# Kernel tuning notes

Measured on AMD Instinct MI355X. Metric: run time of the kernel, lower is better.

Reference implementation:

```python
import jax, jax.numpy as jnp
import numpy as np

EMBED_DIM = 1024
NUM_HEADS = 16
HEAD_DIM = EMBED_DIM // NUM_HEADS


def setup_inputs() -> dict:
    key = jax.random.key(0)
    k_x, k_wqkv, k_bqkv, k_wout, k_bout = jax.random.split(key, 5)
    s = 1.0 / np.sqrt(EMBED_DIM)
    return {
        "x": jax.random.normal(k_x, (2, 2048, EMBED_DIM), dtype=jnp.float32),
        "w_qkv": jax.random.uniform(k_wqkv, (EMBED_DIM, 3 * EMBED_DIM), jnp.float32, -s, s),
        "b_qkv": jax.random.uniform(k_bqkv, (3 * EMBED_DIM,), jnp.float32, -s, s),
        "w_out": jax.random.uniform(k_wout, (EMBED_DIM, EMBED_DIM), jnp.float32, -s, s),
        "b_out": jax.random.uniform(k_bout, (EMBED_DIM,), jnp.float32, -s, s),
    }


def reference(x, w_qkv, b_qkv, w_out, b_out):
    B, S, D = x.shape
    H, Hd = NUM_HEADS, HEAD_DIM
    # qkv projection, then per-head chunk: layout matches torch view(B,S,H,3*Hd).chunk(3,-1)
    qkv = (x @ w_qkv + b_qkv).reshape(B, S, H, 3, Hd)  # [B,S,H,3,Hd]
    q = qkv[..., 0, :]  # [B,S,H,Hd]
    k = qkv[..., 1, :]
    v = qkv[..., 2, :]
    scale = 1.0 / np.sqrt(Hd).astype(np.float32)
    scores = jnp.einsum("bqhd,bkhd->bhqk", q, k) * scale  # [B,H,S,S]
    probs = jax.nn.softmax(scores, axis=-1)
    out = jnp.einsum("bhqk,bkhd->bqhd", probs, v).reshape(B, S, D)
    return out @ w_out + b_out
```

## Files before the change

### kernel.cpp

```cpp
#include <hip/hip_runtime.h>
#include <hip/hip_bf16.h>


typedef __bf16 bf16;
typedef __bf16 bf16x8 __attribute__((ext_vector_type(8)));
typedef float  f32x4  __attribute__((ext_vector_type(4)));
typedef float  f32x16 __attribute__((ext_vector_type(16)));
typedef unsigned int uint;
typedef unsigned int uint2v __attribute__((ext_vector_type(2)));

__device__ __forceinline__ void gload_lds16(const void* g, void* l) {
  __builtin_amdgcn_global_load_lds(
      (const __attribute__((address_space(1))) unsigned int*)g,
      (__attribute__((address_space(3))) unsigned int*)l, 16, 0, 0);
}

__device__ __forceinline__ uint pkbf16(float lo, float hi) {
  union { bf16 h[2]; uint u; } t;
  t.h[0] = (bf16)lo; t.h[1] = (bf16)hi;
  return t.u;
}

__device__ __forceinline__ void pl32swapu(uint& a, uint& b) {
  uint2v r = __builtin_amdgcn_permlane32_swap(a, b, false, false);
  a = r.x; b = r.y;
}
__device__ __forceinline__ void pl32swapf(float& a, float& b) {
  uint ua = __builtin_bit_cast(uint, a), ub = __builtin_bit_cast(uint, b);
  pl32swapu(ua, ub);
  a = __builtin_bit_cast(float, ua); b = __builtin_bit_cast(float, ub);
}

__global__ __launch_bounds__(256) void k_prep(const float* __restrict__ x,
                                              const float* __restrict__ w_qkv,
                                              const float* __restrict__ w_out,
                                              bf16* __restrict__ xb,
                                              bf16* __restrict__ wqT,
                                              bf16* __restrict__ woT) {
  __shared__ float tile[32][33];
  const int b = blockIdx.x;
  const int tid = threadIdx.x;
  if (b < 2048) {
    int i = (b * 256 + tid) * 8;
    float4 a = *(const float4*)(x + i);
    float4 c = *(const float4*)(x + i + 4);
    bf16x8 o;
    o[0] = (bf16)a.x; o[1] = (bf16)a.y; o[2] = (bf16)a.z; o[3] = (bf16)a.w;
    o[4] = (bf16)c.x; o[5] = (bf16)c.y; o[6] = (bf16)c.z; o[7] = (bf16)c.w;
    *(bf16x8*)(xb + i) = o;
    return;
  }
  const bool perm = (b < 5120);
  const float* in = perm ? w_qkv : w_out;
  bf16* out = perm ? wqT : woT;
  const int N = perm ? 3072 : 1024;
  int idx = perm ? (b - 2048) : (b - 5120);
  int gx = perm ? (idx % 96) : (idx % 32);
  int gy = perm ? (idx / 96) : (idx / 32);
  int n0 = gx * 32, k0 = gy * 32;
  int tx = tid & 31, ty = tid >> 5;
#pragma unroll
  for (int i = 0; i < 4; i++)
    tile[ty + i * 8][tx] = in[(size_t)(k0 + ty + i * 8) * N + n0 + tx];
  __syncthreads();
#pragma unroll
  for (int i = 0; i < 4; i++) {
    int n = n0 + ty + i * 8;
    int row = n;
    if (perm) {
      int rem = n % 192;
      row = (rem >> 6) * 1024 + (n / 192) * 64 + (rem & 63);
    }
    out[(size_t)row * 1024 + k0 + tx] = (bf16)tile[tx][ty + i * 8];
  }
}

template<int BM, int BN>
__device__ __forceinline__ void gemm_tile(const bf16* __restrict__ A, const bf16* __restrict__ B,
                                          int K, int m0, int n0,
                                          bf16* As, bf16* Bs, f32x4 acc[BM / 32][BN / 32]) {
  const int tid  = threadIdx.x;
  const int lane = tid & 63;
  const int wr   = (tid >> 7) & 1;
  const int wc   = (tid >> 6) & 1;
  constexpr int LA = BM / 64, LB = BN / 64;
  auto stage = [&](int k0v, int b) {
#pragma unroll
    for (int i = 0; i < LA; i++) {
      int row = i * 64 + (tid >> 2);
      int sw  = (tid & 3) ^ (row & 3);
      gload_lds16(A + (size_t)(m0 + row) * K + k0v + sw * 8, (char*)As + b * (BM * 64) + i * 4096 + tid * 16);
    }
#pragma unroll
    for (int i = 0; i < LB; i++) {
      int row = i * 64 + (tid >> 2);
      int sw  = (tid & 3) ^ (row & 3);
      gload_lds16(B + (size_t)(n0 + row) * K + k0v + sw * 8, (char*)Bs + b * (BN * 64) + i * 4096 + tid * 16);
    }
  };
  const int nk = K / 32;
  stage(0, 0); stage(32, 1); stage(64, 2);
  for (int t = 0; t < nk; t++) {
    if (t < nk - 2) {
      if constexpr (LA + LB == 4) asm volatile("s_waitcnt vmcnt(8)" ::: "memory");
      else                        asm volatile("s_waitcnt vmcnt(6)" ::: "memory");
    } else if (t < nk - 1) {
      if constexpr (LA + LB == 4) asm volatile("s_waitcnt vmcnt(4)" ::: "memory");
      else                        asm volatile("s_waitcnt vmcnt(3)" ::: "memory");
    } else {
      asm volatile("s_waitcnt vmcnt(0)" ::: "memory");
    }
    __builtin_amdgcn_s_barrier();
    asm volatile("" ::: "memory");
    if (t + 3 < nk) stage((t + 3) * 32, (t + 3) & 3);
    const int cur = t & 3;
    bf16x8 af[BM / 32], bfr[BN / 32];
#pragma unroll
    for (int r = 0; r < BM / 32; r++) {
      int ra = wr * (BM / 2) + r * 16 + (lane & 15);
      af[r]  = *(const bf16x8*)((const char*)As + cur * (BM * 64) + ra * 64 + ((((lane >> 4) << 4)) ^ ((ra & 3) << 4)));
    }
#pragma unroll
    for (int c = 0; c < BN / 32; c++) {
      int rb = wc * (BN / 2) + c * 16 + (lane & 15);
      bfr[c] = *(const bf16x8*)((const char*)Bs + cur * (BN * 64) + rb * 64 + ((((lane >> 4) << 4)) ^ ((rb & 3) << 4)));
    }
#pragma unroll
    for (int r = 0; r < BM / 32; r++)
#pragma unroll
      for (int c = 0; c < BN / 32; c++)
        acc[r][c] = __builtin_amdgcn_mfma_f32_16x16x32_bf16(af[r], bfr[c], acc[r][c], 0, 0, 0);
    asm volatile("" ::: "memory");
  }
}

__global__ __launch_bounds__(512, 2) void k_gemm_qkv(const bf16* __restrict__ A, const bf16* __restrict__ Bt,
                                                     const float* __restrict__ bias,
                                                     bf16* __restrict__ qb, bf16* __restrict__ kb,
                                                     bf16* __restrict__ vtb) {
  __shared__ char GS[131072];
  const int tid  = threadIdx.x;
  const int lane = tid & 63;
  const int wave = tid >> 6;
  const int wr   = wave >> 2;
  const int wc   = wave & 3;
  const int m0 = blockIdx.x * 256, n0 = blockIdx.y * 256;
  const int K = 1024;

  f32x4 acc[8][4];
  f32x4 zero = {0.f, 0.f, 0.f, 0.f};
#pragma unroll
  for (int ms = 0; ms < 8; ms++)
#pragma unroll
    for (int ns = 0; ns < 4; ns++) acc[ms][ns] = zero;

  const int ccs = tid & 7;
  int rA[2], rB[2];
  {
    int lr0 = tid >> 3;
    rA[0] = lr0;
    rB[0] = (lr0 & 31) + ((lr0 >> 5) << 6);
    int lr1 = 64 + lr0;
    rA[1] = (lr1 & 63) + 128;
    rB[1] = (lr1 & 31) + ((lr1 >> 5) << 6);
  }
  const bf16* Agp[2]; const bf16* Bgp[2];
  int Alo[2], Blo[2];
#pragma unroll
  for (int j = 0; j < 2; j++) {
    Agp[j] = A  + (size_t)(m0 + rA[j]) * K + (ccs ^ (rA[j] & 7)) * 8;
    Alo[j] = rA[j] * 128 + ccs * 16;
    Bgp[j] = Bt + (size_t)(n0 + rB[j]) * K + (ccs ^ (rB[j] & 7)) * 8;
    Blo[j] = rB[j] * 128 + ccs * 16;
  }
  auto stA = [&](int t, int h) {
    int b = t & 1;
#pragma unroll
    for (int j = 0; j < 2; j++)
      gload_lds16(Agp[j] + (size_t)(h * 64) * K + t * 64, GS + b * 32768 + Alo[j] + h * 8192);
  };
  auto stB = [&](int t, int h) {
    int b = t & 1;
#pragma unroll
    for (int j = 0; j < 2; j++)
      gload_lds16(Bgp[j] + (size_t)(h * 32) * K + t * 64, GS + 65536 + b * 32768 + Blo[j] + h * 4096);
  };

  bf16x8 af[4][2], bf0[2][2], bf1[2][2];
  auto rdA = [&](const char* Ab, int mh) {
#pragma unroll
    for (int ms = 0; ms < 4; ms++)
#pragma unroll
      for (int ks = 0; ks < 2; ks++) {
        int row = wr * 128 + (mh * 4 + ms) * 16 + (lane & 15);
        int ch = (ks * 4 + (lane >> 4)) ^ (row & 7);
        af[ms][ks] = *(const bf16x8*)(Ab + row * 128 + ch * 16);
      }
  };
  auto rdB = [&](const char* Bb, int nh, bf16x8 (&bfx)[2][2]) {
#pragma unroll
    for (int ns = 0; ns < 2; ns++)
#pragma unroll
      for (int ks = 0; ks < 2; ks++) {
        int row = wc * 64 + (nh * 2 + ns) * 16 + (lane & 15);
        int ch = (ks * 4 + (lane >> 4)) ^ (row & 7);
        bfx[ns][ks] = *(const bf16x8*)(Bb + row * 128 + ch * 16);
      }
  };
  auto mm = [&](int mh, int nh, bf16x8 (&bfx)[2][2]) {
    __builtin_amdgcn_s_setprio(1);
#pragma unroll
    for (int ks = 0; ks < 2; ks++)
#pragma unroll
      for (int ms = 0; ms < 4; ms++)
#pragma unroll
        for (int ns = 0; ns < 2; ns++)
          acc[mh * 4 + ms][nh * 2 + ns] =
              __builtin_amdgcn_mfma_f32_16x16x32_bf16(af[ms][ks], bfx[ns][ks],
                                                      acc[mh * 4 + ms][nh * 2 + ns], 0, 0, 0);
    __builtin_amdgcn_s_setprio(0);
  };

#define BARRIER do { asm volatile("" ::: "memory"); __builtin_amdgcn_s_barrier(); \
                     asm volatile("" ::: "memory"); } while (0)

  stA(0, 0); stB(0, 0); stB(0, 1); stA(0, 1);
  stA(1, 0); stB(1, 0); stB(1, 1);
  asm volatile("s_waitcnt vmcnt(6)" ::: "memory");
  __builtin_amdgcn_s_barrier();
  asm volatile("" ::: "memory");

  for (int I = 0; I < 8; I++) {
    const int T = 2 * I;
    const char* Ab0 = GS;
    const char* Bb0 = GS + 65536;
    const char* Ab1 = GS + 32768;
    const char* Bb1 = GS + 65536 + 32768;
    const bool m2 = (T + 2 < 16), m3 = (T + 3 < 16);

    rdA(Ab0, 0); rdB(Bb0, 0, bf0);
    stA(T + 1, 1);
    BARRIER;
    mm(0, 0, bf0);

    rdB(Bb0, 1, bf1);
    if (m2) stA(T + 2, 0);
    BARRIER;
    mm(0, 1, bf1);

    rdA(Ab0, 1);
    if (m2) stB(T + 2, 0);
    BARRIER;
    mm(1, 0, bf0);

    if (m2) {
      stB(T + 2, 1);
      asm volatile("s_waitcnt vmcnt(6)" ::: "memory");
    } else {
      asm volatile("s_waitcnt vmcnt(0)" ::: "memory");
    }
    __builtin_amdgcn_s_barrier();
    asm volatile("" ::: "memory");
    mm(1, 1, bf1);

    rdA(Ab1, 0); rdB(Bb1, 0, bf0);
    if (m2) stA(T + 2, 1);
    BARRIER;
    mm(0, 0, bf0);

    rdB(Bb1, 1, bf1);
    if (m3) stA(T + 3, 0);
    BARRIER;
    mm(0, 1, bf1);

    rdA(Ab1, 1);
    if (m3) stB(T + 3, 0);
    BARRIER;
    mm(1, 0, bf0);

    if (m3) {
      stB(T + 3, 1);
      asm volatile("s_waitcnt vmcnt(6)" ::: "memory");
    } else {
      asm volatile("s_waitcnt vmcnt(0)" ::: "memory");
    }
    __builtin_amdgcn_s_barrier();
    asm volatile("" ::: "memory");
    mm(1, 1, bf1);
  }
#undef BARRIER

  const int group = n0 >> 10;
  const int hb = (n0 & 1023) >> 6;
  const int b_ = m0 >> 11;
  const float QSs = 0.125f * 1.4426950408889634f;
  char* TL = GS;

  if (group < 2) {
#pragma unroll
    for (int ms = 0; ms < 8; ms++) {
      int mloc = wr * 128 + ms * 16 + ((lane >> 4) << 2);
#pragma unroll
      for (int ns = 0; ns < 4; ns++) {
        int nloc = wc * 64 + ns * 16 + (lane & 15);
        int np = n0 + nloc;
        float bv = bias[((np & 1023) >> 6) * 192 + group * 64 + (np & 63)];
#pragma unroll
        for (int g = 0; g < 4; g++) {
          float v = acc[ms][ns][g] + bv;
          if (group == 0) v *= QSs;
          int m = mloc + g;
          int byte = m * 512 + ((((nloc >> 3) ^ (m & 7)) << 4) | ((nloc & 7) << 1));
          *(bf16*)(TL + byte) = (bf16)v;
        }
      }
    }
    __syncthreads();
    bf16* dst = (group == 0) ? qb : kb;
#pragma unroll
    for (int it = 0; it < 16; it++) {
      int cid = it * 512 + tid;
      int row = cid >> 5, cc = cid & 31;
      int hh = hb + (cc >> 3), ck = cc & 7;
      bf16x8 v8 = *(const bf16x8*)(TL + row * 512 + ((cc ^ (row & 7)) << 4));
      *(bf16x8*)(dst + ((size_t)(b_ * 16 + hh) * 2048 + (m0 & 2047) + row) * 64 + ck * 8) = v8;
    }
  } else {
#pragma unroll
    for (int ms = 0; ms < 8; ms++) {
      int mloc = wr * 128 + ms * 16 + ((lane >> 4) << 2);
#pragma unroll
      for (int ns = 0; ns < 4; ns++) {
        int nloc = wc * 64 + ns * 16 + (lane & 15);
        int np = n0 + nloc;
        float bv = bias[((np & 1023) >> 6) * 192 + 2 * 64 + (np & 63)];
#pragma unroll
        for (int g = 0; g < 4; g++) {
          float v = acc[ms][ns][g] + bv;
          int m = mloc + g;
          int byte = nloc * 512 + ((((m >> 3) ^ (nloc & 7)) << 4) | ((m & 7) << 1));
          *(bf16*)(TL + byte) = (bf16)v;
        }
      }
    }
    __syncthreads();
#pragma unroll
    for (int it = 0; it < 16; it++) {
      int cid = it * 512 + tid;
      int row = cid >> 5, mc = cid & 31;
      int hh = hb + (row >> 6), dd = row & 63;
      bf16x8 v8 = *(const bf16x8*)(TL + row * 512 + ((mc ^ (row & 7)) << 4));
      *(bf16x8*)(vtb + ((size_t)(b_ * 16 + hh) * 64 + dd) * 2048 + (m0 & 2047) + mc * 8) = v8;
    }
  }
}

__global__ __launch_bounds__(256) void k_gemm_out(const bf16* __restrict__ A, const bf16* __restrict__ Bt,
                                                  const float* __restrict__ bias,
                                                  float* __restrict__ out) {
  __shared__ bf16 As[4 * 64 * 32];
  __shared__ bf16 Bs[4 * 128 * 32];
  int m0 = blockIdx.x * 64, n0 = blockIdx.y * 128;
  f32x4 zero = {0.f, 0.f, 0.f, 0.f};
  f32x4 acc[2][4];
#pragma unroll
  for (int r = 0; r < 2; r++)
#pragma unroll
    for (int c = 0; c < 4; c++) acc[r][c] = zero;
  gemm_tile<64, 128>(A, Bt, 1024, m0, n0, As, Bs, acc);
  const int lane = threadIdx.x & 63;
  const int wr = (threadIdx.x >> 7) & 1, wc = (threadIdx.x >> 6) & 1;
#pragma unroll
  for (int r = 0; r < 2; r++) {
    int mbase = m0 + wr * 32 + r * 16 + ((lane >> 4) << 2);
#pragma unroll
    for (int c = 0; c < 4; c++) {
      int n = n0 + wc * 64 + c * 16 + (lane & 15);
      float bv = bias[n];
#pragma unroll
      for (int g = 0; g < 4; g++)
        out[(size_t)(mbase + g) * 1024 + n] = acc[r][c][g] + bv;
    }
  }
}

__global__ __launch_bounds__(512, 2) void k_attn(const bf16* __restrict__ qb, const bf16* __restrict__ kb,
                                                 const bf16* __restrict__ vtb, bf16* __restrict__ ob) {
  __shared__ char SMEM[73728];
  const int tid  = threadIdx.x;
  const int lane = tid & 63;
  const int wave = tid >> 6;
  const int qp   = wave & 3;
  const int half = wave >> 2;
  const int ln31 = lane & 31;
  const int g    = lane >> 5;

  int l = blockIdx.x;
  int x = l & 7, j = l >> 3;
  int qt = j & 7;
  int bh = x * 4 + (j >> 3);

  const int q0 = qt * 256 + qp * 64;

  bf16x8 qfa[4], qfb[4];
  {
    const bf16* qpa = qb + ((size_t)bh * 2048 + q0 + ln31) * 64 + g * 8;
    const bf16* qpb = qb + ((size_t)bh * 2048 + q0 + 32 + ln31) * 64 + g * 8;
#pragma unroll
    for (int dc = 0; dc < 4; dc++) {
      qfa[dc] = *(const bf16x8*)(qpa + dc * 16);
      qfb[dc] = *(const bf16x8*)(qpb + dc * 16);
    }
  }

  const f32x16 z16 = 0.f;
  f32x16 Oa0 = 0.f, Oa1 = 0.f, Ob0 = 0.f, Ob1 = 0.f;
  float lacc_a[4] = {0.f, 0.f, 0.f, 0.f};
  float lacc_b[4] = {0.f, 0.f, 0.f, 0.f};

  const int rbo = ln31 * 144 + (g << 4);
  const char* kbs0 = SMEM + half * 9216 + rbo;
  const char* kbs1 = SMEM + 36864 + half * 9216 + rbo;
  const char* vbs0 = SMEM + 18432 + half * 9216 + rbo;
  const char* vbs1 = SMEM + 36864 + 18432 + half * 9216 + rbo;

  const int c1 = tid, r1 = c1 / 9, cc1 = c1 % 9;
  const int of1 = (cc1 == 8 ? 0 : cc1) * 8;
  const bf16* kg0a = kb  + ((size_t)bh * 2048 +        r1) * 64 + of1;
  const bf16* kg1a = kb  + ((size_t)bh * 2048 + 1024 + r1) * 64 + of1;
  const bf16* vg0a = vtb + ((size_t)bh * 64 + r1) * 2048 +        of1;
  const bf16* vg1a = vtb + ((size_t)bh * 64 + r1) * 2048 + 1024 + of1;
  const int se = tid >> 6;
  const int ce = 512 + (tid & 63), re = ce / 9, cce = ce % 9;
  const int ofe = (cce == 8 ? 0 : cce) * 8;
  const bf16* gext =
      (se == 0) ? kb  + ((size_t)bh * 2048 +        re) * 64 + ofe :
      (se == 1) ? kb  + ((size_t)bh * 2048 + 1024 + re) * 64 + ofe :
      (se == 2) ? vtb + ((size_t)bh * 64 + re) * 2048 +        ofe :
                  vtb + ((size_t)bh * 64 + re) * 2048 + 1024 + ofe;
  const size_t gadv = (se < 2) ? 4096 : 64;
  const int eoff = se * 9216 + ce * 16;

  auto stage = [&](int t, int s) {
    char* bs = SMEM + s * 36864;
    gload_lds16(kg0a + (size_t)t * 4096, bs +         c1 * 16);
    gload_lds16(kg1a + (size_t)t * 4096, bs + 9216  + c1 * 16);
    gload_lds16(vg0a + t * 64,           bs + 18432 + c1 * 16);
    gload_lds16(vg1a + t * 64,           bs + 27648 + c1 * 16);
    if (tid < 256) gload_lds16(gext + (size_t)t * gadv, bs + eoff);
  };

  auto smx = [&](f32x16& sv, bf16x8& f0, bf16x8& f1, float (&lc)[4]) {
#pragma unroll
    for (int r = 0; r < 16; r++) sv[r] = __builtin_amdgcn_exp2f(sv[r]);
#pragma unroll
    for (int r = 0; r < 4; r++)
      lc[r] += (sv[r] + sv[r + 4]) + (sv[r + 8] + sv[r + 12]);
    uint a0 = pkbf16(sv[0], sv[1]), a1 = pkbf16(sv[2], sv[3]);
    uint a2 = pkbf16(sv[4], sv[5]), a3 = pkbf16(sv[6], sv[7]);
    pl32swapu(a0, a2); pl32swapu(a1, a3);
    union { uint w[4]; bf16x8 v; } pa;
    pa.w[0] = a0; pa.w[1] = a1; pa.w[2] = a2; pa.w[3] = a3;
    f0 = pa.v;
    uint b0 = pkbf16(sv[8], sv[9]),  b1 = pkbf16(sv[10], sv[11]);
    uint b2 = pkbf16(sv[12], sv[13]), b3 = pkbf16(sv[14], sv[15]);
    pl32swapu(b0, b2); pl32swapu(b1, b3);
    union { uint w[4]; bf16x8 v; } pb;
    pb.w[0] = b0; pb.w[1] = b1; pb.w[2] = b2; pb.w[3] = b3;
    f1 = pb.v;
  };

  stage(0, 0);
  for (int t = 0; t < 16; t++) {
    asm volatile("s_waitcnt vmcnt(0)" ::: "memory");
    __builtin_amdgcn_s_barrier();
    asm volatile("" ::: "memory");
    if (t + 1 < 16) stage(t + 1, (t + 1) & 1);

    const char* Kb = (t & 1) ? kbs1 : kbs0;
    const char* Vb = (t & 1) ? vbs1 : vbs0;

    f32x16 sAa, sAb, sBa, sBb;
    __builtin_amdgcn_s_setprio(1);
    {
      bf16x8 kA = *(const bf16x8*)(Kb + 0);
      bf16x8 kB = *(const bf16x8*)(Kb + 4608);
      sAa = __builtin_amdgcn_mfma_f32_32x32x16_bf16(kA, qfa[0], z16, 0, 0, 0);
      sAb = __builtin_amdgcn_mfma_f32_32x32x16_bf16(kA, qfb[0], z16, 0, 0, 0);
      sBa = __builtin_amdgcn_mfma_f32_32x32x16_bf16(kB, qfa[0], z16, 0, 0, 0);
      sBb = __builtin_amdgcn_mfma_f32_32x32x16_bf16(kB, qfb[0], z16, 0, 0, 0);
    }
#pragma unroll
    for (int dc = 1; dc < 4; dc++) {
      bf16x8 kA = *(const bf16x8*)(Kb + dc * 32);
      bf16x8 kB = *(const bf16x8*)(Kb + 4608 + dc * 32);
      sAa = __builtin_amdgcn_mfma_f32_32x32x16_bf16(kA, qfa[dc], sAa, 0, 0, 0);
      sAb = __builtin_amdgcn_mfma_f32_32x32x16_bf16(kA, qfb[dc], sAb, 0, 0, 0);
      sBa = __builtin_amdgcn_mfma_f32_32x32x16_bf16(kB, qfa[dc], sBa, 0, 0, 0);
      sBb = __builtin_amdgcn_mfma_f32_32x32x16_bf16(kB, qfb[dc], sBb, 0, 0, 0);
    }
    __builtin_amdgcn_s_setprio(0);

    bf16x8 fa0, fa1, fb0, fb1;
    smx(sAa, fa0, fa1, lacc_a);
    smx(sAb, fb0, fb1, lacc_b);
    __builtin_amdgcn_s_setprio(1);
    {
      bf16x8 v0 = *(const bf16x8*)(Vb + 0);
      bf16x8 v1 = *(const bf16x8*)(Vb + 4608);
      Oa0 = __builtin_amdgcn_mfma_f32_32x32x16_bf16(v0, fa0, Oa0, 0, 0, 0);
      Ob0 = __builtin_amdgcn_mfma_f32_32x32x16_bf16(v0, fb0, Ob0, 0, 0, 0);
      Oa1 = __builtin_amdgcn_mfma_f32_32x32x16_bf16(v1, fa0, Oa1, 0, 0, 0);
      Ob1 = __builtin_amdgcn_mfma_f32_32x32x16_bf16(v1, fb0, Ob1, 0, 0, 0);
      v0 = *(const bf16x8*)(Vb + 32);
      v1 = *(const bf16x8*)(Vb + 4640);
      Oa0 = __builtin_amdgcn_mfma_f32_32x32x16_bf16(v0, fa1, Oa0, 0, 0, 0);
      Ob0 = __builtin_amdgcn_mfma_f32_32x32x16_bf16(v0, fb1, Ob0, 0, 0, 0);
      Oa1 = __builtin_amdgcn_mfma_f32_32x32x16_bf16(v1, fa1, Oa1, 0, 0, 0);
      Ob1 = __builtin_amdgcn_mfma_f32_32x32x16_bf16(v1, fb1, Ob1, 0, 0, 0);
    }
    __builtin_amdgcn_s_setprio(0);
    smx(sBa, fa0, fa1, lacc_a);
    smx(sBb, fb0, fb1, lacc_b);
    __builtin_amdgcn_s_setprio(1);
    {
      bf16x8 v0 = *(const bf16x8*)(Vb + 64);
      bf16x8 v1 = *(const bf16x8*)(Vb + 4672);
      Oa0 = __builtin_amdgcn_mfma_f32_32x32x16_bf16(v0, fa0, Oa0, 0, 0, 0);
      Ob0 = __builtin_amdgcn_mfma_f32_32x32x16_bf16(v0, fb0, Ob0, 0, 0, 0);
      Oa1 = __builtin_amdgcn_mfma_f32_32x32x16_bf16(v1, fa0, Oa1, 0, 0, 0);
      Ob1 = __builtin_amdgcn_mfma_f32_32x32x16_bf16(v1, fb0, Ob1, 0, 0, 0);
      v0 = *(const bf16x8*)(Vb + 96);
      v1 = *(const bf16x8*)(Vb + 4704);
      Oa0 = __builtin_amdgcn_mfma_f32_32x32x16_bf16(v0, fa1, Oa0, 0, 0, 0);
      Ob0 = __builtin_amdgcn_mfma_f32_32x32x16_bf16(v0, fb1, Ob0, 0, 0, 0);
      Oa1 = __builtin_amdgcn_mfma_f32_32x32x16_bf16(v1, fa1, Oa1, 0, 0, 0);
      Ob1 = __builtin_amdgcn_mfma_f32_32x32x16_bf16(v1, fb1, Ob1, 0, 0, 0);
    }
    __builtin_amdgcn_s_setprio(0);
    asm volatile("" ::: "memory");
  }

  float l_ra = (lacc_a[0] + lacc_a[1]) + (lacc_a[2] + lacc_a[3]);
  { float o = l_ra; pl32swapf(l_ra, o); l_ra += o; }
  float l_rb = (lacc_b[0] + lacc_b[1]) + (lacc_b[2] + lacc_b[3]);
  { float o = l_rb; pl32swapf(l_rb, o); l_rb += o; }

  float* Opart = (float*)SMEM;
  float* LsA   = (float*)(SMEM + 69632);
  float* LsB   = (float*)(SMEM + 70144);
  __syncthreads();
  if (half == 1) {
    float* my = Opart + (qp * 64 + lane) * 68;
#pragma unroll
    for (int c = 0; c < 4; c++) {
      *(f32x4*)(my +      c * 4) = f32x4{Oa0[c*4], Oa0[c*4+1], Oa0[c*4+2], Oa0[c*4+3]};
      *(f32x4*)(my + 16 + c * 4) = f32x4{Oa1[c*4], Oa1[c*4+1], Oa1[c*4+2], Oa1[c*4+3]};
      *(f32x4*)(my + 32 + c * 4) = f32x4{Ob0[c*4], Ob0[c*4+1], Ob0[c*4+2], Ob0[c*4+3]};
      *(f32x4*)(my + 48 + c * 4) = f32x4{Ob1[c*4], Ob1[c*4+1], Ob1[c*4+2], Ob1[c*4+3]};
    }
    if (lane < 32) { LsA[qp * 32 + ln31] = l_ra; LsB[qp * 32 + ln31] = l_rb; }
  }
  __syncthreads();
  float inva = 0.f, invb = 0.f;
  if (half == 0) {
    const float* pr = Opart + (qp * 64 + lane) * 68;
#pragma unroll
    for (int c = 0; c < 4; c++) {
      f32x4 a0 = *(const f32x4*)(pr +      c * 4);
      f32x4 a1 = *(const f32x4*)(pr + 16 + c * 4);
      f32x4 b0 = *(const f32x4*)(pr + 32 + c * 4);
      f32x4 b1 = *(const f32x4*)(pr + 48 + c * 4);
#pragma unroll
      for (int k = 0; k < 4; k++) {
        Oa0[c*4+k] += a0[k]; Oa1[c*4+k] += a1[k];
        Ob0[c*4+k] += b0[k]; Ob1[c*4+k] += b1[k];
      }
    }
    inva = 1.0f / (l_ra + LsA[qp * 32 + ln31]);
    invb = 1.0f / (l_rb + LsB[qp * 32 + ln31]);
  }
  __syncthreads();
  bf16 (*Os)[64][72] = reinterpret_cast<bf16 (*)[64][72]>(SMEM);
  if (half == 0) {
#pragma unroll
    for (int r = 0; r < 16; r++) {
      int d0 = (r & 3) + 8 * (r >> 2) + 4 * g;
      Os[qp][ln31][d0]           = (bf16)(Oa0[r] * inva);
      Os[qp][ln31][d0 + 32]      = (bf16)(Oa1[r] * inva);
      Os[qp][32 + ln31][d0]      = (bf16)(Ob0[r] * invb);
      Os[qp][32 + ln31][d0 + 32] = (bf16)(Ob1[r] * invb);
    }
  }
  __syncthreads();
  {
    int b_ = bh >> 4, h = bh & 15;
#pragma unroll
    for (int it = 0; it < 4; it++) {
      int cid = it * 512 + tid;
      int row256 = cid >> 3, c = cid & 7;
      int qpp = row256 >> 6, row = row256 & 63;
      bf16x8 v8o = *(const bf16x8*)&Os[qpp][row][c * 8];
      *(bf16x8*)(ob + ((size_t)(b_ * 2048 + qt * 256 + qpp * 64 + row)) * 1024 + h * 64 + c * 8) = v8o;
    }
  }
}

extern "C" void kernel_launch(void* const* d_in, const int* in_sizes, int n_in,
                              void* d_out, int out_size, void* d_ws, size_t ws_size,
                              hipStream_t stream) {
  const float* x     = (const float*)d_in[0];
  const float* w_qkv = (const float*)d_in[1];
  const float* b_qkv = (const float*)d_in[2];
  const float* w_out = (const float*)d_in[3];
  const float* b_out = (const float*)d_in[4];
  float* out = (float*)d_out;

  char* ws = (char*)d_ws;
  bf16* xb  = (bf16*)ws;
  bf16* wqT = (bf16*)(ws + (8ull  << 20));
  bf16* woT = (bf16*)(ws + (14ull << 20));
  bf16* qb  = (bf16*)(ws + (16ull << 20));
  bf16* kb  = (bf16*)(ws + (24ull << 20));
  bf16* vtb = (bf16*)(ws + (32ull << 20));

  k_prep<<<6144, 256, 0, stream>>>(x, w_qkv, w_out, xb, wqT, woT);
  k_gemm_qkv<<<dim3(16, 12), 512, 0, stream>>>(xb, wqT, b_qkv, qb, kb, vtb);
  k_attn<<<256, 512, 0, stream>>>(qb, kb, vtb, xb);
  k_gemm_out<<<dim3(64, 8), 256, 0, stream>>>(xb, woT, b_out, out);
}
```

Baseline: 103.9 us.

## Triple-buffer attention K/V with deferred PV for upper waves; swizzle GEMM block order

Result: no change. 104.7 us (+0.8%).

```diff
diff --git a/kernel.cpp b/kernel.cpp
--- a/kernel.cpp
+++ b/kernel.cpp
@@ -144,7 +144,9 @@
   const int wave = tid >> 6;
   const int wr   = wave >> 2;
   const int wc   = wave & 3;
-  const int m0 = blockIdx.x * 256, n0 = blockIdx.y * 256;
+  const int l = blockIdx.x;
+  const int swz = (l & 7) * 24 + (l >> 3);
+  const int m0 = (swz / 12) * 256, n0 = (swz % 12) * 256;
   const int K = 1024;
 
   f32x4 acc[8][4];
@@ -360,7 +362,9 @@
                                                   float* __restrict__ out) {
   __shared__ bf16 As[4 * 64 * 32];
   __shared__ bf16 Bs[4 * 128 * 32];
-  int m0 = blockIdx.x * 64, n0 = blockIdx.y * 128;
+  const int l = blockIdx.x;
+  const int swz = (l & 7) * 64 + (l >> 3);
+  int m0 = (swz >> 3) * 64, n0 = (swz & 7) * 128;
   f32x4 zero = {0.f, 0.f, 0.f, 0.f};
   f32x4 acc[2][4];
 #pragma unroll
@@ -386,7 +390,7 @@
 
 __global__ __launch_bounds__(512, 2) void k_attn(const bf16* __restrict__ qb, const bf16* __restrict__ kb,
                                                  const bf16* __restrict__ vtb, bf16* __restrict__ ob) {
-  __shared__ char SMEM[73728];
+  __shared__ char SMEM[147456];
   const int tid  = threadIdx.x;
   const int lane = tid & 63;
   const int wave = tid >> 6;
@@ -419,10 +423,8 @@
   float lacc_b[4] = {0.f, 0.f, 0.f, 0.f};
 
   const int rbo = ln31 * 144 + (g << 4);
-  const char* kbs0 = SMEM + half * 9216 + rbo;
-  const char* kbs1 = SMEM + 36864 + half * 9216 + rbo;
-  const char* vbs0 = SMEM + 18432 + half * 9216 + rbo;
-  const char* vbs1 = SMEM + 36864 + 18432 + half * 9216 + rbo;
+  const char* kbs = SMEM + half * 9216 + rbo;
+  const char* vbs = SMEM + 18432 + half * 9216 + rbo;
 
   const int c1 = tid, r1 = c1 / 9, cc1 = c1 % 9;
   const int of1 = (cc1 == 8 ? 0 : cc1) * 8;
@@ -470,15 +472,45 @@
     f1 = pb.v;
   };
 
+  auto pv_chunk = [&](const char* Vb, int cb, bf16x8 f0a, bf16x8 f1a, bf16x8 f0b, bf16x8 f1b) {
+    bf16x8 v0 = *(const bf16x8*)(Vb + cb);
+    bf16x8 v1 = *(const bf16x8*)(Vb + 4608 + cb);
+    Oa0 = __builtin_amdgcn_mfma_f32_32x32x16_bf16(v0, f0a, Oa0, 0, 0, 0);
+    Ob0 = __builtin_amdgcn_mfma_f32_32x32x16_bf16(v0, f0b, Ob0, 0, 0, 0);
+    Oa1 = __builtin_amdgcn_mfma_f32_32x32x16_bf16(v1, f0a, Oa1, 0, 0, 0);
+    Ob1 = __builtin_amdgcn_mfma_f32_32x32x16_bf16(v1, f0b, Ob1, 0, 0, 0);
+    v0 = *(const bf16x8*)(Vb + cb + 32);
+    v1 = *(const bf16x8*)(Vb + 4608 + cb + 32);
+    Oa0 = __builtin_amdgcn_mfma_f32_32x32x16_bf16(v0, f1a, Oa0, 0, 0, 0);
+    Ob0 = __builtin_amdgcn_mfma_f32_32x32x16_bf16(v0, f1b, Ob0, 0, 0, 0);
+    Oa1 = __builtin_amdgcn_mfma_f32_32x32x16_bf16(v1, f1a, Oa1, 0, 0, 0);
+    Ob1 = __builtin_amdgcn_mfma_f32_32x32x16_bf16(v1, f1b, Ob1, 0, 0, 0);
+  };
+
+  bf16x8 hf0a, hf1a, hf0b, hf1b;
+
   stage(0, 0);
+  stage(1, 1);
   for (int t = 0; t < 16; t++) {
-    asm volatile("s_waitcnt vmcnt(0)" ::: "memory");
+    if (t + 1 < 16) {
+      if (wave < 4) asm volatile("s_waitcnt vmcnt(5)" ::: "memory");
+      else          asm volatile("s_waitcnt vmcnt(4)" ::: "memory");
+    } else {
+      asm volatile("s_waitcnt vmcnt(0)" ::: "memory");
+    }
     __builtin_amdgcn_s_barrier();
     asm volatile("" ::: "memory");
-    if (t + 1 < 16) stage(t + 1, (t + 1) & 1);
-
-    const char* Kb = (t & 1) ? kbs1 : kbs0;
-    const char* Vb = (t & 1) ? vbs1 : vbs0;
+    if (t + 2 < 16) stage(t + 2, (t + 2) & 3);
+
+    const char* Kb = kbs + (t & 3) * 36864;
+    const char* Vb = vbs + (t & 3) * 36864;
+
+    if (half && t) {
+      const char* Vp = vbs + ((t + 3) & 3) * 36864;
+      __builtin_amdgcn_s_setprio(1);
+      pv_chunk(Vp, 64, hf0a, hf1a, hf0b, hf1b);
+      __builtin_amdgcn_s_setprio(0);
+    }
 
     f32x16 sAa, sAb, sBa, sBb;
     __builtin_amdgcn_s_setprio(1);
@@ -505,40 +537,22 @@
     smx(sAa, fa0, fa1, lacc_a);
     smx(sAb, fb0, fb1, lacc_b);
     __builtin_amdgcn_s_setprio(1);
-    {
-      bf16x8 v0 = *(const bf16x8*)(Vb + 0);
-      bf16x8 v1 = *(const bf16x8*)(Vb + 4608);
-      Oa0 = __builtin_amdgcn_mfma_f32_32x32x16_bf16(v0, fa0, Oa0, 0, 0, 0);
-      Ob0 = __builtin_amdgcn_mfma_f32_32x32x16_bf16(v0, fb0, Ob0, 0, 0, 0);
-      Oa1 = __builtin_amdgcn_mfma_f32_32x32x16_bf16(v1, fa0, Oa1, 0, 0, 0);
-      Ob1 = __builtin_amdgcn_mfma_f32_32x32x16_bf16(v1, fb0, Ob1, 0, 0, 0);
-      v0 = *(const bf16x8*)(Vb + 32);
-      v1 = *(const bf16x8*)(Vb + 4640);
-      Oa0 = __builtin_amdgcn_mfma_f32_32x32x16_bf16(v0, fa1, Oa0, 0, 0, 0);
-      Ob0 = __builtin_amdgcn_mfma_f32_32x32x16_bf16(v0, fb1, Ob0, 0, 0, 0);
-      Oa1 = __builtin_amdgcn_mfma_f32_32x32x16_bf16(v1, fa1, Oa1, 0, 0, 0);
-      Ob1 = __builtin_amdgcn_mfma_f32_32x32x16_bf16(v1, fb1, Ob1, 0, 0, 0);
-    }
+    pv_chunk(Vb, 0, fa0, fa1, fb0, fb1);
     __builtin_amdgcn_s_setprio(0);
-    smx(sBa, fa0, fa1, lacc_a);
-    smx(sBb, fb0, fb1, lacc_b);
-    __builtin_amdgcn_s_setprio(1);
-    {
-      bf16x8 v0 = *(const bf16x8*)(Vb + 64);
-      bf16x8 v1 = *(const bf16x8*)(Vb + 4672);
-      Oa0 = __builtin_amdgcn_mfma_f32_32x32x16_bf16(v0, fa0, Oa0, 0, 0, 0);
-      Ob0 = __builtin_amdgcn_mfma_f32_32x32x16_bf16(v0, fb0, Ob0, 0, 0, 0);
-      Oa1 = __builtin_amdgcn_mfma_f32_32x32x16_bf16(v1, fa0, Oa1, 0, 0, 0);
-      Ob1 = __builtin_amdgcn_mfma_f32_32x32x16_bf16(v1, fb0, Ob1, 0, 0, 0);
-      v0 = *(const bf16x8*)(Vb + 96);
-      v1 = *(const bf16x8*)(Vb + 4704);
-      Oa0 = __builtin_amdgcn_mfma_f32_32x32x16_bf16(v0, fa1, Oa0, 0, 0, 0);
-      Ob0 = __builtin_amdgcn_mfma_f32_32x32x16_bf16(v0, fb1, Ob0, 0, 0, 0);
-      Oa1 = __builtin_amdgcn_mfma_f32_32x32x16_bf16(v1, fa1, Oa1, 0, 0, 0);
-      Ob1 = __builtin_amdgcn_mfma_f32_32x32x16_bf16(v1, fb1, Ob1, 0, 0, 0);
-    }
-    __builtin_amdgcn_s_setprio(0);
+    if (half) {
+      smx(sBa, hf0a, hf1a, lacc_a);
+      smx(sBb, hf0b, hf1b, lacc_b);
+    } else {
+      smx(sBa, fa0, fa1, lacc_a);
+      smx(sBb, fb0, fb1, lacc_b);
+      __builtin_amdgcn_s_setprio(1);
+      pv_chunk(Vb, 64, fa0, fa1, fb0, fb1);
+      __builtin_amdgcn_s_setprio(0);
+    }
     asm volatile("" ::: "memory");
+  }
+  if (half) {
+    pv_chunk(vbs + 3 * 36864, 64, hf0a, hf1a, hf0b, hf1b);
   }
 
   float l_ra = (lacc_a[0] + lacc_a[1]) + (lacc_a[2] + lacc_a[3]);
@@ -625,7 +639,7 @@
   bf16* vtb = (bf16*)(ws + (32ull << 20));
 
   k_prep<<<6144, 256, 0, stream>>>(x, w_qkv, w_out, xb, wqT, woT);
-  k_gemm_qkv<<<dim3(16, 12), 512, 0, stream>>>(xb, wqT, b_qkv, qb, kb, vtb);
+  k_gemm_qkv<<<192, 512, 0, stream>>>(xb, wqT, b_qkv, qb, kb, vtb);
   k_attn<<<256, 512, 0, stream>>>(qb, kb, vtb, xb);
-  k_gemm_out<<<dim3(64, 8), 256, 0, stream>>>(xb, woT, b_out, out);
-}
+  k_gemm_out<<<512, 256, 0, stream>>>(xb, woT, b_out, out);
+}
```
